# Performance work log

Hardware: AMD Instinct MI355X
Metric: run time of the kernel (lower is better)

The kernel has to match this reference:

```python
import jax, jax.numpy as jnp
import numpy as np

V, E, B = 40000, 240000, 8
HID, LAT, TDIM, NL = 128, 64, 16, 4

def _w(k, shape):
    fan_in = shape[-2] if len(shape) >= 2 else 1
    return jax.random.normal(k, shape, dtype=jnp.float32) / jnp.sqrt(jnp.float32(fan_in))

def setup_inputs() -> dict:
    key = jax.random.key(0)
    ks = jax.random.split(key, 24)
    inp = {
        'pos': jax.random.normal(ks[0], (V, 3), dtype=jnp.float32),
        't': jax.random.uniform(ks[1], (B,), dtype=jnp.float32),
        'z': jax.random.normal(ks[2], (B, LAT), dtype=jnp.float32),
        'edge_index': jax.random.randint(ks[3], (2, E), 0, V, dtype=jnp.int64),
        'batch': jax.random.randint(ks[4], (V,), 0, B, dtype=jnp.int64),
        # time_embed: Linear(1,16) -> SiLU -> Linear(16,16)
        'te_w1': _w(ks[5], (1, TDIM)), 'te_b1': jnp.zeros((TDIM,), jnp.float32),
        'te_w2': _w(ks[6], (TDIM, TDIM)), 'te_b2': jnp.zeros((TDIM,), jnp.float32),
        # cond_proj: Linear(latent+time, hidden)
        'cp_w': _w(ks[7], (LAT + TDIM, HID)), 'cp_b': jnp.zeros((HID,), jnp.float32),
        # EGNN layers (stacked over n_layers)
        'We1': _w(ks[8], (NL, 2 * HID + 1, HID)), 'be1': jnp.zeros((NL, HID), jnp.float32),
        'We2': _w(ks[9], (NL, HID, HID)), 'be2': jnp.zeros((NL, HID), jnp.float32),
        'Wc1': _w(ks[10], (NL, HID, HID)), 'bc1': jnp.zeros((NL, HID), jnp.float32),
        'Wc2': _w(ks[11], (NL, HID, 1)),
        'Wn1': _w(ks[12], (NL, 2 * HID, HID)), 'bn1': jnp.zeros((NL, HID), jnp.float32),
        'Wn2': _w(ks[13], (NL, HID, HID)), 'bn2': jnp.zeros((NL, HID), jnp.float32),
    }
    return inp

def reference(pos, t, z, edge_index, batch,
              te_w1, te_b1, te_w2, te_b2, cp_w, cp_b,
              We1, be1, We2, be2, Wc1, bc1, Wc2, Wn1, bn1, Wn2, bn2):
    silu = jax.nn.silu
    # conditioning: per-node time embedding + latent code -> h (V, HID)
    t_node = t[batch][:, None]                      # (V,1)
    t_emb = silu(t_node @ te_w1 + te_b1) @ te_w2 + te_b2   # (V, TDIM)
    h = jnp.concatenate([z[batch], t_emb], axis=-1) @ cp_w + cp_b  # (V, HID)

    row, col = edge_index[0], edge_index[1]
    x = pos
    for l in range(NL):
        rel = x[row] - x[col]                       # (E,3)
        d2 = jnp.sum(rel * rel, axis=-1, keepdims=True)  # (E,1)
        e_in = jnp.concatenate([h[row], h[col], d2], axis=-1)  # (E, 2H+1)
        m = silu(silu(e_in @ We1[l] + be1[l]) @ We2[l] + be2[l])  # (E,H)
        coef = silu(m @ Wc1[l] + bc1[l]) @ Wc2[l]   # (E,1)
        x = x + jax.ops.segment_sum(rel * coef, row, num_segments=V)
        agg = jax.ops.segment_sum(m, row, num_segments=V)  # (V,H)
        n_in = jnp.concatenate([h, agg], axis=-1)
        h = h + silu(n_in @ Wn1[l] + bn1[l]) @ Wn2[l] + bn2[l]
    velocity = x - pos
    return velocity
```

## Files before the change

kernel.cpp:

```cpp
#include <hip/hip_runtime.h>

#define HID 128
#define NLAY 4

typedef float f32x4 __attribute__((ext_vector_type(4)));
typedef short bf16x8 __attribute__((ext_vector_type(8)));

union FragU { uint4 u; bf16x8 v; };

__device__ __forceinline__ float silu_f(float x) {
  return x / (1.0f + __expf(-x));
}

__device__ __forceinline__ unsigned int pack_pair(float x) {
  unsigned int bx = __float_as_uint(x);
  unsigned int hi = bx & 0xffff0000u;
  float lof = x - __uint_as_float(hi);
  return (bx >> 16) | (__float_as_uint(lof) & 0xffff0000u);
}

__device__ __forceinline__ float unpack_sum(unsigned int p) {
  return __uint_as_float(p << 16) + __uint_as_float(p & 0xffff0000u);
}

__device__ __forceinline__ void unpack_frags(const uint4& a, const uint4& b,
                                             FragU& hi, FragU& lo) {
  hi.u.x = __builtin_amdgcn_perm(a.y, a.x, 0x05040100u);
  hi.u.y = __builtin_amdgcn_perm(a.w, a.z, 0x05040100u);
  hi.u.z = __builtin_amdgcn_perm(b.y, b.x, 0x05040100u);
  hi.u.w = __builtin_amdgcn_perm(b.w, b.z, 0x05040100u);
  lo.u.x = __builtin_amdgcn_perm(a.y, a.x, 0x07060302u);
  lo.u.y = __builtin_amdgcn_perm(a.w, a.z, 0x07060302u);
  lo.u.z = __builtin_amdgcn_perm(b.y, b.x, 0x07060302u);
  lo.u.w = __builtin_amdgcn_perm(b.w, b.z, 0x07060302u);
}

__device__ __forceinline__ void pack8(const float* uu, FragU& hi, FragU& lo) {
  unsigned int h[8], l[8];
  #pragma unroll
  for (int i = 0; i < 8; ++i) {
    unsigned int b = __float_as_uint(uu[i]);
    h[i] = b >> 16;
    float lof = uu[i] - __uint_as_float(b & 0xffff0000u);
    l[i] = __float_as_uint(lof) >> 16;
  }
  hi.u.x = h[0] | (h[1] << 16);
  hi.u.y = h[2] | (h[3] << 16);
  hi.u.z = h[4] | (h[5] << 16);
  hi.u.w = h[6] | (h[7] << 16);
  lo.u.x = l[0] | (l[1] << 16);
  lo.u.y = l[2] | (l[3] << 16);
  lo.u.z = l[4] | (l[5] << 16);
  lo.u.w = l[6] | (l[7] << 16);
}

__global__ void wprep_kernel(const float* __restrict__ W, unsigned short* __restrict__ out) {
  int id = blockIdx.x * 256 + threadIdx.x;
  if (id >= 16384) return;
  int i = id & 7;
  int lane = (id >> 3) & 63;
  int obkb = id >> 9;
  int k = (obkb >> 3) * 32 + ((lane >> 4) << 3) + i;
  int col = (obkb & 7) * 16 + (lane & 15);
  float x = W[k * 128 + col];
  unsigned int bx = __float_as_uint(x);
  unsigned int hi = bx & 0xffff0000u;
  float lof = x - __uint_as_float(hi);
  out[id] = (unsigned short)(bx >> 16);
  out[16384 + id] = (unsigned short)(__float_as_uint(lof) >> 16);
}

__global__ void hb_kernel(const float* __restrict__ t, const float* __restrict__ z,
                          const float* __restrict__ te_w1, const float* __restrict__ te_b1,
                          const float* __restrict__ te_w2, const float* __restrict__ te_b2,
                          const float* __restrict__ cp_w, const float* __restrict__ cp_b,
                          float* __restrict__ hb) {
  int b = blockIdx.x;
  int j = threadIdx.x;
  float tv = t[b];
  float e1[16];
  #pragma unroll
  for (int i = 0; i < 16; ++i) e1[i] = silu_f(tv * te_w1[i] + te_b1[i]);
  float acc = cp_b[j];
  for (int i = 0; i < 64; ++i) acc += z[b*64 + i] * cp_w[i*HID + j];
  #pragma unroll
  for (int i = 0; i < 16; ++i) {
    float te = te_b2[i];
    #pragma unroll
    for (int k = 0; k < 16; ++k) te += e1[k] * te_w2[k*16 + i];
    acc += te * cp_w[(64 + i)*HID + j];
  }
  hb[b*HID + j] = acc;
}

__global__ void scatter_h_kernel(const int* __restrict__ batch, const float* __restrict__ hb,
                                 float* __restrict__ h, int V) {
  int idx = blockIdx.x * blockDim.x + threadIdx.x;
  if (idx < V * 32) {
    int v = idx >> 5, c = idx & 31;
    int b = batch[v];
    ((float4*)h)[(size_t)v*32 + c] = ((const float4*)hb)[b*32 + c];
  }
}

__global__ void packx_kernel(const float* __restrict__ pos, float4* __restrict__ x4, int V) {
  int v = blockIdx.x * blockDim.x + threadIdx.x;
  if (v < V) x4[v] = make_float4(pos[3*v], pos[3*v+1], pos[3*v+2], 0.f);
}

__global__ void hist_kernel(const int* __restrict__ rowp, int* __restrict__ cnt, int E) {
  int e = blockIdx.x * blockDim.x + threadIdx.x;
  if (e < E) atomicAdd(&cnt[rowp[e]], 1);
}

__global__ void scan_kernel(const int* __restrict__ cnt, int* __restrict__ offp, int V) {
  __shared__ int s[1024];
  __shared__ int carry_s;
  int tid = threadIdx.x;
  if (tid == 0) carry_s = 0;
  __syncthreads();
  for (int base = 0; base < V; base += 1024) {
    int v = base + tid;
    int val = (v < V) ? cnt[v] : 0;
    s[tid] = val;
    __syncthreads();
    for (int d = 1; d < 1024; d <<= 1) {
      int tval = (tid >= d) ? s[tid - d] : 0;
      __syncthreads();
      s[tid] += tval;
      __syncthreads();
    }
    int c0 = carry_s;
    if (v < V) offp[v] = c0 + s[tid] - val;
    int tot = s[1023];
    __syncthreads();
    if (tid == 0) carry_s = c0 + tot;
    __syncthreads();
  }
  if (tid == 0) offp[V] = carry_s;
}

__global__ void scatter_perm_kernel(const int* __restrict__ rowp, const int* __restrict__ colp,
                                    const int* __restrict__ offp, int* __restrict__ fill,
                                    int* __restrict__ srow, int* __restrict__ scol, int E) {
  int e = blockIdx.x * blockDim.x + threadIdx.x;
  if (e < E) {
    int r = rowp[e];
    int p = offp[r] + atomicAdd(&fill[r], 1);
    srow[p] = r;
    scol[p] = colp[e];
  }
}

template<int MODE>
__global__ __launch_bounds__(512, 2) void ngemm_kernel(
    const float* __restrict__ in, const unsigned short* __restrict__ wfr,
    const float* __restrict__ bias, const float* __restrict__ addsrc,
    float* __restrict__ out, int V)
{
  extern __shared__ uint4 ldsB[];
  for (int i = threadIdx.x; i < 4096; i += 512) ldsB[i] = ((const uint4*)wfr)[i];
  __syncthreads();
  const int tid = threadIdx.x;
  const int wave = tid >> 6, lane = tid & 63;
  const int g = lane >> 4, c16 = lane & 15;
  float bias_r[8];
  if (MODE == 1 || MODE == 3) {
    #pragma unroll
    for (int ob = 0; ob < 8; ++ob) bias_r[ob] = bias[ob*16 + c16];
  }
  const int gw = blockIdx.x*8 + wave;
  const int nw = gridDim.x*8;
  const int ntiles = V >> 5;
  for (int tt = gw; tt < ntiles; tt += nw) {
    int vb = tt << 5;
    int rowA0 = vb + c16, rowA1 = vb + 16 + c16;
    f32x4 zero4 = {0.f, 0.f, 0.f, 0.f};
    f32x4 acc[2][8];
    #pragma unroll
    for (int s = 0; s < 2; ++s)
      #pragma unroll
      for (int ob = 0; ob < 8; ++ob) acc[s][ob] = zero4;
    #pragma unroll
    for (int kb = 0; kb < 4; ++kb) {
      int ch0 = kb*32 + g*8;
      FragU Ah[2], Al[2];
      #pragma unroll
      for (int s = 0; s < 2; ++s) {
        const float4* pr = (const float4*)(in + (size_t)(s ? rowA1 : rowA0)*HID + ch0);
        float4 a0 = pr[0], a1 = pr[1];
        float uu[8] = {a0.x, a0.y, a0.z, a0.w, a1.x, a1.y, a1.z, a1.w};
        pack8(uu, Ah[s], Al[s]);
      }
      #pragma unroll
      for (int ob = 0; ob < 8; ++ob) {
        FragU Bh, Bl;
        Bh.u = ldsB[(kb*8 + ob)*64 + lane];
        Bl.u = ldsB[2048 + (kb*8 + ob)*64 + lane];
        #pragma unroll
        for (int s = 0; s < 2; ++s) {
          acc[s][ob] = __builtin_amdgcn_mfma_f32_16x16x32_bf16(Al[s].v, Bh.v, acc[s][ob], 0, 0, 0);
          acc[s][ob] = __builtin_amdgcn_mfma_f32_16x16x32_bf16(Ah[s].v, Bl.v, acc[s][ob], 0, 0, 0);
          acc[s][ob] = __builtin_amdgcn_mfma_f32_16x16x32_bf16(Ah[s].v, Bh.v, acc[s][ob], 0, 0, 0);
        }
      }
    }
    #pragma unroll
    for (int s = 0; s < 2; ++s)
      #pragma unroll
      for (int ob = 0; ob < 8; ++ob)
        #pragma unroll
        for (int r = 0; r < 4; ++r) {
          int v = vb + s*16 + 4*g + r;
          size_t idx = (size_t)v*HID + ob*16 + c16;
          float val = acc[s][ob][r];
          if (MODE == 0) out[idx] = val;
          if (MODE == 1) out[idx] = val + bias_r[ob];
          if (MODE == 2) out[idx] = silu_f(val + addsrc[idx]);
          if (MODE == 3) out[idx] += val + bias_r[ob];
        }
  }
}

__global__ __launch_bounds__(512, 2) void edge_fused_kernel(
    const int* __restrict__ srow, const int* __restrict__ scol,
    const float4* __restrict__ x4,
    const float* __restrict__ p1, const float* __restrict__ p2,
    const unsigned short* __restrict__ wfrE2, const unsigned short* __restrict__ wfrC1,
    const float* __restrict__ wd2_l, const float* __restrict__ be2_l,
    const float* __restrict__ bc1_l, const float* __restrict__ Wc2_l,
    unsigned int* __restrict__ m_pairs, float4* __restrict__ rc_ws, int E)
{
  extern __shared__ uint4 lds[];
  uint4* ldsB = lds;
  unsigned int* ldsT = (unsigned int*)(lds + 8192);
  for (int i = threadIdx.x; i < 4096; i += 512) ldsB[i] = ((const uint4*)wfrE2)[i];
  for (int i = threadIdx.x; i < 4096; i += 512) ldsB[4096 + i] = ((const uint4*)wfrC1)[i];
  __syncthreads();
  const int tid = threadIdx.x;
  const int wave = tid >> 6, lane = tid & 63;
  const int g = lane >> 4, c16 = lane & 15;
  unsigned int* myT = ldsT + wave*1024;
  float be2_r[8], bc1_r[8], wc2_r[8];
  #pragma unroll
  for (int ob = 0; ob < 8; ++ob) {
    be2_r[ob] = be2_l[ob*16 + c16];
    bc1_r[ob] = bc1_l[ob*16 + c16];
    wc2_r[ob] = Wc2_l[ob*16 + c16];
  }
  const int swz = (c16 & 7) << 2;
  const int gw = blockIdx.x*8 + wave;
  const int nw = gridDim.x*8;
  const int ntiles = E >> 5;
  for (int tt = gw; tt < ntiles; tt += nw) {
    int ib = tt << 5;
    int r_[2], c_[2]; float d2_[2], rlx[2], rly[2], rlz[2];
    #pragma unroll
    for (int s = 0; s < 2; ++s) {
      int i = ib + s*16 + c16;
      r_[s] = srow[i]; c_[s] = scol[i];
      float4 xr = x4[r_[s]], xc = x4[c_[s]];
      rlx[s] = xr.x-xc.x; rly[s] = xr.y-xc.y; rlz[s] = xr.z-xc.z;
      d2_[s] = rlx[s]*rlx[s] + rly[s]*rly[s] + rlz[s]*rlz[s];
    }
    f32x4 zero4 = {0.f, 0.f, 0.f, 0.f};
    f32x4 acc[2][8];
    #pragma unroll
    for (int s = 0; s < 2; ++s)
      #pragma unroll
      for (int ob = 0; ob < 8; ++ob) acc[s][ob] = zero4;
    #pragma unroll
    for (int kb = 0; kb < 4; ++kb) {
      int ch0 = kb*32 + g*8;
      float4 w0 = *(const float4*)(wd2_l + ch0);
      float4 w1 = *(const float4*)(wd2_l + ch0 + 4);
      FragU Ah[2], Al[2];
      #pragma unroll
      for (int s = 0; s < 2; ++s) {
        const float4* pr1 = (const float4*)(p1 + (size_t)r_[s]*HID + ch0);
        const float4* pr2 = (const float4*)(p2 + (size_t)c_[s]*HID + ch0);
        float4 a0 = pr1[0], a1 = pr1[1];
        float4 b0 = pr2[0], b1 = pr2[1];
        float d2 = d2_[s];
        float uu[8];
        uu[0] = silu_f(a0.x + b0.x + d2*w0.x);
        uu[1] = silu_f(a0.y + b0.y + d2*w0.y);
        uu[2] = silu_f(a0.z + b0.z + d2*w0.z);
        uu[3] = silu_f(a0.w + b0.w + d2*w0.w);
        uu[4] = silu_f(a1.x + b1.x + d2*w1.x);
        uu[5] = silu_f(a1.y + b1.y + d2*w1.y);
        uu[6] = silu_f(a1.z + b1.z + d2*w1.z);
        uu[7] = silu_f(a1.w + b1.w + d2*w1.w);
        pack8(uu, Ah[s], Al[s]);
      }
      #pragma unroll
      for (int ob = 0; ob < 8; ++ob) {
        FragU Bh, Bl;
        Bh.u = ldsB[(kb*8 + ob)*64 + lane];
        Bl.u = ldsB[2048 + (kb*8 + ob)*64 + lane];
        #pragma unroll
        for (int s = 0; s < 2; ++s) {
          acc[s][ob] = __builtin_amdgcn_mfma_f32_16x16x32_bf16(Al[s].v, Bh.v, acc[s][ob], 0, 0, 0);
          acc[s][ob] = __builtin_amdgcn_mfma_f32_16x16x32_bf16(Ah[s].v, Bl.v, acc[s][ob], 0, 0, 0);
          acc[s][ob] = __builtin_amdgcn_mfma_f32_16x16x32_bf16(Ah[s].v, Bh.v, acc[s][ob], 0, 0, 0);
        }
      }
    }
    #pragma unroll
    for (int s = 0; s < 2; ++s) {
      f32x4 acc2[8];
      #pragma unroll
      for (int ob = 0; ob < 8; ++ob) acc2[ob] = zero4;
      #pragma unroll
      for (int p = 0; p < 2; ++p) {
        #pragma unroll
        for (int ob4 = 0; ob4 < 4; ++ob4) {
          int ob = p*4 + ob4;
          #pragma unroll
          for (int r = 0; r < 4; ++r) {
            int row = 4*g + r;
            float mval = silu_f(acc[s][ob][r] + be2_r[ob]);
            myT[(row << 6) + ((ob4*16 + c16) ^ ((row & 7) << 2))] = pack_pair(mval);
          }
        }
        unsigned int* gout = m_pairs + (size_t)(ib + s*16)*HID + p*64;
        #pragma unroll
        for (int inst = 0; inst < 4; ++inst) {
          int flat = inst*256 + lane*4;
          int row = flat >> 6, col = flat & 63;
          uint4 vv = *(const uint4*)&myT[(row << 6) + (col ^ ((row & 7) << 2))];
          *(uint4*)(gout + (size_t)row*HID + col) = vv;
        }
        #pragma unroll
        for (int kbl = 0; kbl < 2; ++kbl) {
          int kb = p*2 + kbl;
          int col0 = kbl*32 + g*8;
          uint4 a = *(const uint4*)&myT[(c16 << 6) + (col0 ^ swz)];
          uint4 b = *(const uint4*)&myT[(c16 << 6) + ((col0 + 4) ^ swz)];
          FragU Ah, Al;
          unpack_frags(a, b, Ah, Al);
          #pragma unroll
          for (int ob = 0; ob < 8; ++ob) {
            FragU Bh, Bl;
            Bh.u = ldsB[4096 + (kb*8 + ob)*64 + lane];
            Bl.u = ldsB[6144 + (kb*8 + ob)*64 + lane];
            acc2[ob] = __builtin_amdgcn_mfma_f32_16x16x32_bf16(Al.v, Bh.v, acc2[ob], 0, 0, 0);
            acc2[ob] = __builtin_amdgcn_mfma_f32_16x16x32_bf16(Ah.v, Bl.v, acc2[ob], 0, 0, 0);
            acc2[ob] = __builtin_amdgcn_mfma_f32_16x16x32_bf16(Ah.v, Bh.v, acc2[ob], 0, 0, 0);
          }
        }
      }
      float part[4] = {0.f, 0.f, 0.f, 0.f};
      #pragma unroll
      for (int ob = 0; ob < 8; ++ob)
        #pragma unroll
        for (int r = 0; r < 4; ++r) {
          float tv = silu_f(acc2[ob][r] + bc1_r[ob]);
          part[r] += tv * wc2_r[ob];
        }
      #pragma unroll
      for (int r = 0; r < 4; ++r) {
        #pragma unroll
        for (int m = 1; m < 16; m <<= 1) part[r] += __shfl_xor(part[r], m);
      }
      #pragma unroll
      for (int r = 0; r < 4; ++r) {
        float sx = __shfl(rlx[s], 4*g + r);
        float sy = __shfl(rly[s], 4*g + r);
        float sz = __shfl(rlz[s], 4*g + r);
        if (c16 == 0) {
          float cf = part[r];
          rc_ws[ib + s*16 + 4*g + r] = make_float4(sx*cf, sy*cf, sz*cf, 0.f);
        }
      }
    }
  }
}

__global__ void agg_kernel(const int* __restrict__ offp,
                           const unsigned int* __restrict__ m_pairs,
                           const float4* __restrict__ rc_ws,
                           float* __restrict__ agg, float4* __restrict__ x4, int V)
{
  int wave = threadIdx.x >> 6, lane = threadIdx.x & 63;
  int v = blockIdx.x*4 + wave;
  if (v >= V) return;
  int s = offp[v], e = offp[v+1];
  float acc0 = 0.f, acc1 = 0.f;
  float rx = 0.f, ry = 0.f, rz = 0.f;
  for (int i = s; i < e; ++i) {
    uint2 mv = ((const uint2*)m_pairs)[(size_t)i*64 + lane];
    acc0 += unpack_sum(mv.x);
    acc1 += unpack_sum(mv.y);
    float4 rc = rc_ws[i];
    rx += rc.x; ry += rc.y; rz += rc.z;
  }
  ((float2*)agg)[(size_t)v*64 + lane] = make_float2(acc0, acc1);
  if (lane == 0) {
    float4 xv = x4[v];
    xv.x += rx; xv.y += ry; xv.z += rz;
    x4[v] = xv;
  }
}

__global__ void vel_kernel(const float4* __restrict__ x4, const float* __restrict__ pos,
                           float* __restrict__ out, int V) {
  int v = blockIdx.x * blockDim.x + threadIdx.x;
  if (v < V) {
    float4 xv = x4[v];
    out[3*v]   = xv.x - pos[3*v];
    out[3*v+1] = xv.y - pos[3*v+1];
    out[3*v+2] = xv.z - pos[3*v+2];
  }
}

extern "C" void kernel_launch(void* const* d_in, const int* in_sizes, int n_in,
                              void* d_out, int out_size, void* d_ws, size_t ws_size,
                              hipStream_t stream) {
  const float* pos   = (const float*)d_in[0];
  const float* t     = (const float*)d_in[1];
  const float* z     = (const float*)d_in[2];
  const int*   ei    = (const int*)d_in[3];
  const int*   batch = (const int*)d_in[4];
  const float* te_w1 = (const float*)d_in[5];
  const float* te_b1 = (const float*)d_in[6];
  const float* te_w2 = (const float*)d_in[7];
  const float* te_b2 = (const float*)d_in[8];
  const float* cp_w  = (const float*)d_in[9];
  const float* cp_b  = (const float*)d_in[10];
  const float* We1   = (const float*)d_in[11];
  const float* be1   = (const float*)d_in[12];
  const float* We2   = (const float*)d_in[13];
  const float* be2   = (const float*)d_in[14];
  const float* Wc1   = (const float*)d_in[15];
  const float* bc1   = (const float*)d_in[16];
  const float* Wc2   = (const float*)d_in[17];
  const float* Wn1   = (const float*)d_in[18];
  const float* bn1   = (const float*)d_in[19];
  const float* Wn2   = (const float*)d_in[20];
  const float* bn2   = (const float*)d_in[21];

  const int V = in_sizes[4];
  const int E = in_sizes[3] / 2;
  const int* rowp = ei;
  const int* colp = ei + E;

  char* base = (char*)d_ws;
  size_t off_b = 0;
  auto alloc = [&](size_t bytes) -> char* {
    char* p = base + off_b;
    off_b += (bytes + 255) & ~(size_t)255;
    return p;
  };
  float*  h     = (float*) alloc((size_t)V*HID*4);
  float*  pA    = (float*) alloc((size_t)V*HID*4);
  float*  pB    = (float*) alloc((size_t)V*HID*4);
  float4* x4    = (float4*)alloc((size_t)V*16);
  char*   m_buf = alloc((size_t)E*HID*4);
  float4* rc_ws = (float4*)alloc((size_t)E*16);
  float*  hb    = (float*) alloc(8*HID*4);
  int*    cnt   = (int*)   alloc((size_t)V*4);
  int*    offp  = (int*)   alloc((size_t)(V+1)*4);
  int*    fill  = (int*)   alloc((size_t)V*4);
  int*    srow  = (int*)   alloc((size_t)E*4);
  int*    scol  = (int*)   alloc((size_t)E*4);
  unsigned short* wfrag = (unsigned short*)alloc((size_t)NLAY*7*32768*sizeof(unsigned short));
  (void)ws_size; (void)n_in; (void)out_size;

  unsigned int* m_pairs = (unsigned int*)m_buf;
  float* q_buf = (float*)m_buf;

  auto wf = [&](int l, int j) -> unsigned short* {
    return wfrag + ((size_t)(l*7 + j))*32768;
  };

  const int NLDS = 65536;
  const int FLDS = 163840;
  hipFuncSetAttribute((const void*)ngemm_kernel<0>, hipFuncAttributeMaxDynamicSharedMemorySize, NLDS);
  hipFuncSetAttribute((const void*)ngemm_kernel<1>, hipFuncAttributeMaxDynamicSharedMemorySize, NLDS);
  hipFuncSetAttribute((const void*)ngemm_kernel<2>, hipFuncAttributeMaxDynamicSharedMemorySize, NLDS);
  hipFuncSetAttribute((const void*)ngemm_kernel<3>, hipFuncAttributeMaxDynamicSharedMemorySize, NLDS);
  hipFuncSetAttribute((const void*)edge_fused_kernel, hipFuncAttributeMaxDynamicSharedMemorySize, FLDS);

  hb_kernel<<<8, 128, 0, stream>>>(t, z, te_w1, te_b1, te_w2, te_b2, cp_w, cp_b, hb);
  scatter_h_kernel<<<(V*32 + 255)/256, 256, 0, stream>>>(batch, hb, h, V);
  packx_kernel<<<(V + 255)/256, 256, 0, stream>>>(pos, x4, V);
  hipMemsetAsync(cnt, 0, (size_t)V*4, stream);
  hipMemsetAsync(fill, 0, (size_t)V*4, stream);
  hist_kernel<<<(E + 255)/256, 256, 0, stream>>>(rowp, cnt, E);
  scan_kernel<<<1, 1024, 0, stream>>>(cnt, offp, V);
  scatter_perm_kernel<<<(E + 255)/256, 256, 0, stream>>>(rowp, colp, offp, fill, srow, scol, E);

  for (int l = 0; l < NLAY; ++l) {
    wprep_kernel<<<64, 256, 0, stream>>>(We1 + (size_t)l*257*HID,            wf(l,0));
    wprep_kernel<<<64, 256, 0, stream>>>(We1 + (size_t)l*257*HID + 128*HID,  wf(l,1));
    wprep_kernel<<<64, 256, 0, stream>>>(We2 + (size_t)l*HID*HID,            wf(l,2));
    wprep_kernel<<<64, 256, 0, stream>>>(Wc1 + (size_t)l*HID*HID,            wf(l,3));
    wprep_kernel<<<64, 256, 0, stream>>>(Wn1 + (size_t)l*256*HID,            wf(l,4));
    wprep_kernel<<<64, 256, 0, stream>>>(Wn1 + (size_t)l*256*HID + 128*HID,  wf(l,5));
    wprep_kernel<<<64, 256, 0, stream>>>(Wn2 + (size_t)l*HID*HID,            wf(l,6));
  }

  const int ngrid = ((V >> 5) + 7) / 8;
  const int egrid = 256;

  for (int l = 0; l < NLAY; ++l) {
    const float* wd2_l = We1 + (size_t)l*257*HID + 256*HID;
    const float* Wc2_l = Wc2 + (size_t)l*HID;
    const float* be1_l = be1 + l*HID;
    const float* be2_l = be2 + l*HID;
    const float* bc1_l = bc1 + l*HID;
    const float* bn1_l = bn1 + l*HID;
    const float* bn2_l = bn2 + l*HID;

    ngemm_kernel<1><<<ngrid, 512, NLDS, stream>>>(h, wf(l,0), be1_l, nullptr, pA, V);
    ngemm_kernel<0><<<ngrid, 512, NLDS, stream>>>(h, wf(l,1), nullptr, nullptr, pB, V);
    edge_fused_kernel<<<egrid, 512, FLDS, stream>>>(srow, scol, x4, pA, pB,
                                                    wf(l,2), wf(l,3), wd2_l, be2_l,
                                                    bc1_l, Wc2_l, m_pairs, rc_ws, E);
    agg_kernel<<<(V + 3)/4, 256, 0, stream>>>(offp, m_pairs, rc_ws, pB, x4, V);
    ngemm_kernel<1><<<ngrid, 512, NLDS, stream>>>(h, wf(l,4), bn1_l, nullptr, pA, V);
    ngemm_kernel<2><<<ngrid, 512, NLDS, stream>>>(pB, wf(l,5), nullptr, pA, q_buf, V);
    ngemm_kernel<3><<<ngrid, 512, NLDS, stream>>>(q_buf, wf(l,6), bn2_l, nullptr, h, V);
  }
  vel_kernel<<<(V + 255)/256, 256, 0, stream>>>(x4, pos, (float*)d_out, V);
}
```

Before: 1.442 ms.

## Fuse paired node GEMMs into dual-weight kernels and use rcp in SiLU

Replaces the two per-layer node projections of h (the row and col halves of We1) with one kernel that loads both weight halves into LDS and reads h once. It also fuses the two halves of the node-update first layer (h and agg) into a single accumulating kernel that applies bias and SiLU directly, removing the intermediate q buffer pass. SiLU now uses a hardware reciprocal instead of a divide. The cost is double the LDS per block (128 KB, one block per CU) and a per-wave tile of 16 rows instead of the previous tiling, which may lower occupancy. The reciprocal may also slightly change numerics.

```diff
diff --git a/kernel.cpp b/kernel.cpp
--- a/kernel.cpp
+++ b/kernel.cpp
@@ -9,7 +9,8 @@
 union FragU { uint4 u; bf16x8 v; };
 
 __device__ __forceinline__ float silu_f(float x) {
-  return x / (1.0f + __expf(-x));
+  float e = __expf(-x);
+  return x * __builtin_amdgcn_rcpf(1.0f + e);
 }
 
 __device__ __forceinline__ unsigned int pack_pair(float x) {
@@ -149,6 +150,134 @@
     int p = offp[r] + atomicAdd(&fill[r], 1);
     srow[p] = r;
     scol[p] = colp[e];
+  }
+}
+
+__global__ __launch_bounds__(512, 1) void pgemm_kernel(
+    const float* __restrict__ in,
+    const unsigned short* __restrict__ wfrT, const unsigned short* __restrict__ wfrB,
+    const float* __restrict__ be1_l,
+    float* __restrict__ p1, float* __restrict__ p2, int V)
+{
+  extern __shared__ uint4 ldsB[];
+  for (int i = threadIdx.x; i < 4096; i += 512) ldsB[i] = ((const uint4*)wfrT)[i];
+  for (int i = threadIdx.x; i < 4096; i += 512) ldsB[4096 + i] = ((const uint4*)wfrB)[i];
+  __syncthreads();
+  const int tid = threadIdx.x;
+  const int wave = tid >> 6, lane = tid & 63;
+  const int g = lane >> 4, c16 = lane & 15;
+  float be1_r[8];
+  #pragma unroll
+  for (int ob = 0; ob < 8; ++ob) be1_r[ob] = be1_l[ob*16 + c16];
+  const int gw = blockIdx.x*8 + wave;
+  const int nw = gridDim.x*8;
+  const int ntiles = V >> 4;
+  for (int tt = gw; tt < ntiles; tt += nw) {
+    int vb = tt << 4;
+    int rowA = vb + c16;
+    f32x4 zero4 = {0.f, 0.f, 0.f, 0.f};
+    f32x4 accT[8], accB[8];
+    #pragma unroll
+    for (int ob = 0; ob < 8; ++ob) { accT[ob] = zero4; accB[ob] = zero4; }
+    #pragma unroll
+    for (int kb = 0; kb < 4; ++kb) {
+      int ch0 = kb*32 + g*8;
+      FragU Ah, Al;
+      const float4* pr = (const float4*)(in + (size_t)rowA*HID + ch0);
+      float4 a0 = pr[0], a1 = pr[1];
+      float uu[8] = {a0.x, a0.y, a0.z, a0.w, a1.x, a1.y, a1.z, a1.w};
+      pack8(uu, Ah, Al);
+      #pragma unroll
+      for (int ob = 0; ob < 8; ++ob) {
+        FragU BhT, BlT, BhB, BlB;
+        BhT.u = ldsB[(kb*8 + ob)*64 + lane];
+        BlT.u = ldsB[2048 + (kb*8 + ob)*64 + lane];
+        BhB.u = ldsB[4096 + (kb*8 + ob)*64 + lane];
+        BlB.u = ldsB[6144 + (kb*8 + ob)*64 + lane];
+        accT[ob] = __builtin_amdgcn_mfma_f32_16x16x32_bf16(Al.v, BhT.v, accT[ob], 0, 0, 0);
+        accT[ob] = __builtin_amdgcn_mfma_f32_16x16x32_bf16(Ah.v, BlT.v, accT[ob], 0, 0, 0);
+        accT[ob] = __builtin_amdgcn_mfma_f32_16x16x32_bf16(Ah.v, BhT.v, accT[ob], 0, 0, 0);
+        accB[ob] = __builtin_amdgcn_mfma_f32_16x16x32_bf16(Al.v, BhB.v, accB[ob], 0, 0, 0);
+        accB[ob] = __builtin_amdgcn_mfma_f32_16x16x32_bf16(Ah.v, BlB.v, accB[ob], 0, 0, 0);
+        accB[ob] = __builtin_amdgcn_mfma_f32_16x16x32_bf16(Ah.v, BhB.v, accB[ob], 0, 0, 0);
+      }
+    }
+    #pragma unroll
+    for (int ob = 0; ob < 8; ++ob)
+      #pragma unroll
+      for (int r = 0; r < 4; ++r) {
+        int v = vb + 4*g + r;
+        size_t idx = (size_t)v*HID + ob*16 + c16;
+        p1[idx] = accT[ob][r] + be1_r[ob];
+        p2[idx] = accB[ob][r];
+      }
+  }
+}
+
+__global__ __launch_bounds__(512, 1) void nu1_kernel(
+    const float* __restrict__ h, const float* __restrict__ agg,
+    const unsigned short* __restrict__ wfrT, const unsigned short* __restrict__ wfrB,
+    const float* __restrict__ bn1_l, float* __restrict__ q, int V)
+{
+  extern __shared__ uint4 ldsB[];
+  for (int i = threadIdx.x; i < 4096; i += 512) ldsB[i] = ((const uint4*)wfrT)[i];
+  for (int i = threadIdx.x; i < 4096; i += 512) ldsB[4096 + i] = ((const uint4*)wfrB)[i];
+  __syncthreads();
+  const int tid = threadIdx.x;
+  const int wave = tid >> 6, lane = tid & 63;
+  const int g = lane >> 4, c16 = lane & 15;
+  float bn1_r[8];
+  #pragma unroll
+  for (int ob = 0; ob < 8; ++ob) bn1_r[ob] = bn1_l[ob*16 + c16];
+  const int gw = blockIdx.x*8 + wave;
+  const int nw = gridDim.x*8;
+  const int ntiles = V >> 4;
+  for (int tt = gw; tt < ntiles; tt += nw) {
+    int vb = tt << 4;
+    int rowA = vb + c16;
+    f32x4 zero4 = {0.f, 0.f, 0.f, 0.f};
+    f32x4 acc[8];
+    #pragma unroll
+    for (int ob = 0; ob < 8; ++ob) acc[ob] = zero4;
+    #pragma unroll
+    for (int kb = 0; kb < 4; ++kb) {
+      int ch0 = kb*32 + g*8;
+      FragU Ah, Al, Gh, Gl;
+      {
+        const float4* pr = (const float4*)(h + (size_t)rowA*HID + ch0);
+        float4 a0 = pr[0], a1 = pr[1];
+        float uu[8] = {a0.x, a0.y, a0.z, a0.w, a1.x, a1.y, a1.z, a1.w};
+        pack8(uu, Ah, Al);
+      }
+      {
+        const float4* pr = (const float4*)(agg + (size_t)rowA*HID + ch0);
+        float4 a0 = pr[0], a1 = pr[1];
+        float uu[8] = {a0.x, a0.y, a0.z, a0.w, a1.x, a1.y, a1.z, a1.w};
+        pack8(uu, Gh, Gl);
+      }
+      #pragma unroll
+      for (int ob = 0; ob < 8; ++ob) {
+        FragU BhT, BlT, BhB, BlB;
+        BhT.u = ldsB[(kb*8 + ob)*64 + lane];
+        BlT.u = ldsB[2048 + (kb*8 + ob)*64 + lane];
+        BhB.u = ldsB[4096 + (kb*8 + ob)*64 + lane];
+        BlB.u = ldsB[6144 + (kb*8 + ob)*64 + lane];
+        acc[ob] = __builtin_amdgcn_mfma_f32_16x16x32_bf16(Al.v, BhT.v, acc[ob], 0, 0, 0);
+        acc[ob] = __builtin_amdgcn_mfma_f32_16x16x32_bf16(Ah.v, BlT.v, acc[ob], 0, 0, 0);
+        acc[ob] = __builtin_amdgcn_mfma_f32_16x16x32_bf16(Ah.v, BhT.v, acc[ob], 0, 0, 0);
+        acc[ob] = __builtin_amdgcn_mfma_f32_16x16x32_bf16(Gl.v, BhB.v, acc[ob], 0, 0, 0);
+        acc[ob] = __builtin_amdgcn_mfma_f32_16x16x32_bf16(Gh.v, BlB.v, acc[ob], 0, 0, 0);
+        acc[ob] = __builtin_amdgcn_mfma_f32_16x16x32_bf16(Gh.v, BhB.v, acc[ob], 0, 0, 0);
+      }
+    }
+    #pragma unroll
+    for (int ob = 0; ob < 8; ++ob)
+      #pragma unroll
+      for (int r = 0; r < 4; ++r) {
+        int v = vb + 4*g + r;
+        size_t idx = (size_t)v*HID + ob*16 + c16;
+        q[idx] = silu_f(acc[ob][r] + bn1_r[ob]);
+      }
   }
 }
 
@@ -468,18 +597,17 @@
   (void)ws_size; (void)n_in; (void)out_size;
 
   unsigned int* m_pairs = (unsigned int*)m_buf;
-  float* q_buf = (float*)m_buf;
 
   auto wf = [&](int l, int j) -> unsigned short* {
     return wfrag + ((size_t)(l*7 + j))*32768;
   };
 
   const int NLDS = 65536;
+  const int PLDS = 131072;
   const int FLDS = 163840;
-  hipFuncSetAttribute((const void*)ngemm_kernel<0>, hipFuncAttributeMaxDynamicSharedMemorySize, NLDS);
-  hipFuncSetAttribute((const void*)ngemm_kernel<1>, hipFuncAttributeMaxDynamicSharedMemorySize, NLDS);
-  hipFuncSetAttribute((const void*)ngemm_kernel<2>, hipFuncAttributeMaxDynamicSharedMemorySize, NLDS);
-  hipFuncSetAttribute((const void*)ngemm_kernel<3>, hipFuncAttributeMaxDynamicSharedMemorySize, NLDS);
+  hipFuncSetAttribute((const void*)pgemm_kernel,      hipFuncAttributeMaxDynamicSharedMemorySize, PLDS);
+  hipFuncSetAttribute((const void*)nu1_kernel,        hipFuncAttributeMaxDynamicSharedMemorySize, PLDS);
+  hipFuncSetAttribute((const void*)ngemm_kernel<3>,   hipFuncAttributeMaxDynamicSharedMemorySize, NLDS);
   hipFuncSetAttribute((const void*)edge_fused_kernel, hipFuncAttributeMaxDynamicSharedMemorySize, FLDS);
 
   hb_kernel<<<8, 128, 0, stream>>>(t, z, te_w1, te_b1, te_w2, te_b2, cp_w, cp_b, hb);
@@ -501,6 +629,7 @@
     wprep_kernel<<<64, 256, 0, stream>>>(Wn2 + (size_t)l*HID*HID,            wf(l,6));
   }
 
+  const int pgrid = ((V >> 4) + 7) / 8;
   const int ngrid = ((V >> 5) + 7) / 8;
   const int egrid = 256;
 
@@ -513,15 +642,13 @@
     const float* bn1_l = bn1 + l*HID;
     const float* bn2_l = bn2 + l*HID;
 
-    ngemm_kernel<1><<<ngrid, 512, NLDS, stream>>>(h, wf(l,0), be1_l, nullptr, pA, V);
-    ngemm_kernel<0><<<ngrid, 512, NLDS, stream>>>(h, wf(l,1), nullptr, nullptr, pB, V);
+    pgemm_kernel<<<pgrid, 512, PLDS, stream>>>(h, wf(l,0), wf(l,1), be1_l, pA, pB, V);
     edge_fused_kernel<<<egrid, 512, FLDS, stream>>>(srow, scol, x4, pA, pB,
                                                     wf(l,2), wf(l,3), wd2_l, be2_l,
                                                     bc1_l, Wc2_l, m_pairs, rc_ws, E);
     agg_kernel<<<(V + 3)/4, 256, 0, stream>>>(offp, m_pairs, rc_ws, pB, x4, V);
-    ngemm_kernel<1><<<ngrid, 512, NLDS, stream>>>(h, wf(l,4), bn1_l, nullptr, pA, V);
-    ngemm_kernel<2><<<ngrid, 512, NLDS, stream>>>(pB, wf(l,5), nullptr, pA, q_buf, V);
-    ngemm_kernel<3><<<ngrid, 512, NLDS, stream>>>(q_buf, wf(l,6), bn2_l, nullptr, h, V);
+    nu1_kernel<<<pgrid, 512, PLDS, stream>>>(h, pB, wf(l,4), wf(l,5), bn1_l, pA, V);
+    ngemm_kernel<3><<<ngrid, 512, NLDS, stream>>>(pA, wf(l,6), bn2_l, nullptr, h, V);
   }
   vel_kernel<<<(V + 255)/256, 256, 0, stream>>>(x4, pos, (float*)d_out, V);
 }
```

After: 1.937 ms. 1.34x slower.
